# Kernel tuning notes

Hardware: AMD Instinct MI355X
Metric: run time of the kernel (lower is better)

Reference implementation:

```python
import jax, jax.numpy as jnp
import numpy as np

B, S, D, H, HD, L, W, MLP = 1, 4096, 1024, 16, 64, 3, 512, 4096
NB = S // W
EPS = 1e-5

def _layer_norm(x, g, b):
    m = jnp.mean(x, axis=-1, keepdims=True)
    v = jnp.mean(jnp.square(x - m), axis=-1, keepdims=True)
    return (x - m) * jax.lax.rsqrt(v + EPS) * g + b

def _rotate_half(x):
    x1, x2 = jnp.split(x, 2, axis=-1)
    return jnp.concatenate([-x2, x1], axis=-1)

def setup_inputs() -> dict:
    key = jax.random.key(0)
    ks = jax.random.split(key, 12)
    def nrm(k, shape):
        return jax.random.normal(k, shape, jnp.float32) * 0.02
    return {
        'hidden_states': jax.random.normal(ks[0], (B, S, D), jnp.float32),
        'position_ids': jnp.broadcast_to(jnp.arange(S, dtype=jnp.int32), (B, S)),
        'ln1_g': jnp.ones((L, D), jnp.float32), 'ln1_b': jnp.zeros((L, D), jnp.float32),
        'wq': nrm(ks[1], (L, D, D)), 'bq': jnp.zeros((L, D), jnp.float32),
        'wk': nrm(ks[2], (L, D, D)), 'bk': jnp.zeros((L, D), jnp.float32),
        'wv': nrm(ks[3], (L, D, D)), 'bv': jnp.zeros((L, D), jnp.float32),
        'wo': nrm(ks[4], (L, D, D)), 'bo': jnp.zeros((L, D), jnp.float32),
        'ln2_g': jnp.ones((L, D), jnp.float32), 'ln2_b': jnp.zeros((L, D), jnp.float32),
        'w1': nrm(ks[5], (L, D, MLP)), 'b1': jnp.zeros((L, MLP), jnp.float32),
        'w2': nrm(ks[6], (L, MLP, D)), 'b2': jnp.zeros((L, D), jnp.float32),
        'fln_g': jnp.ones((D,), jnp.float32), 'fln_b': jnp.zeros((D,), jnp.float32),
    }

def reference(hidden_states, position_ids, ln1_g, ln1_b, wq, bq, wk, bk, wv, bv,
              wo, bo, ln2_g, ln2_b, w1, b1, w2, b2, fln_g, fln_b):
    # RoPE tables (half-split / LLaMA convention)
    inv_freq = 1.0 / (10000.0 ** (jnp.arange(0, HD, 2, dtype=jnp.float32) / HD))
    ang = position_ids.astype(jnp.float32)[..., None] * inv_freq          # [B,S,HD/2]
    cos = jnp.concatenate([jnp.cos(ang)] * 2, axis=-1)[:, :, None, :]     # [B,S,1,HD]
    sin = jnp.concatenate([jnp.sin(ang)] * 2, axis=-1)[:, :, None, :]

    # causal sliding-window mask over (query-in-block, key-in-2-blocks)
    qi = jnp.arange(W)[:, None]
    kj = jnp.arange(2 * W)[None, :]
    rel = qi + W - kj                                                     # = i - j globally
    base = (rel >= 0) & (rel < W)                                         # [W,2W]
    valid = jnp.ones((NB, 2 * W), bool).at[0, :W].set(False)              # no keys before t=0
    mask = base[None, :, :] & valid[:, None, :]                           # [NB,W,2W]
    scale = HD ** -0.5

    x = hidden_states
    for l in range(L):
        h = _layer_norm(x, ln1_g[l], ln1_b[l])
        q = (h @ wq[l] + bq[l]).reshape(B, S, H, HD)
        k = (h @ wk[l] + bk[l]).reshape(B, S, H, HD)
        v = (h @ wv[l] + bv[l]).reshape(B, S, H, HD)
        q = q * cos + _rotate_half(q) * sin
        k = k * cos + _rotate_half(k) * sin
        qb = q.reshape(B, NB, W, H, HD)
        # keys/values for block b = [block b-1, block b] (pad one block in front)
        kp = jnp.pad(k, ((0, 0), (W, 0), (0, 0), (0, 0)))
        vp = jnp.pad(v, ((0, 0), (W, 0), (0, 0), (0, 0)))
        k2 = jnp.concatenate([kp[:, :-W].reshape(B, NB, W, H, HD),
                              kp[:, W:].reshape(B, NB, W, H, HD)], axis=2)  # [B,NB,2W,H,HD]
        v2 = jnp.concatenate([vp[:, :-W].reshape(B, NB, W, H, HD),
                              vp[:, W:].reshape(B, NB, W, H, HD)], axis=2)
        s = jnp.einsum('bnqhd,bnkhd->bnhqk', qb, k2) * scale              # [B,NB,H,W,2W]
        s = jnp.where(mask[None, :, None, :, :], s, -1e30)
        a = jax.nn.softmax(s, axis=-1)
        o = jnp.einsum('bnhqk,bnkhd->bnqhd', a, v2).reshape(B, S, D)
        x = x + (o @ wo[l] + bo[l])
        h = _layer_norm(x, ln2_g[l], ln2_b[l])
        m = jax.nn.gelu(h @ w1[l] + b1[l], approximate=False) @ w2[l] + b2[l]
        x = x + m
    return _layer_norm(x, fln_g, fln_b)
```

## Files before the change

### kernel.cpp

```cpp
#include <hip/hip_runtime.h>

typedef unsigned short u16;
typedef short s8v __attribute__((ext_vector_type(8)));
typedef float f4v __attribute__((ext_vector_type(4)));

__device__ __forceinline__ float bf2f(u16 u){ return __uint_as_float(((unsigned)u)<<16); }
__device__ __forceinline__ u16 f2bf(float f){
  unsigned u = __float_as_uint(f);
  unsigned r = u + 0x7fffu + ((u>>16)&1u);
  return (u16)(r>>16);
}
__device__ __forceinline__ void gload16(const void* g, void* l){
  __builtin_amdgcn_global_load_lds((const __attribute__((address_space(1))) void*)g,
                                   (__attribute__((address_space(3))) void*)l, 16, 0, 0);
}

struct TJobs {
  const float* src[18];
  u16* dst[18];
  int R[18];
  int C[18];
  int start[19];
};

__global__ __launch_bounds__(256) void transpose_pack(TJobs jb){
  __shared__ float tile[32][33];
  int bid = blockIdx.x;
  int j = 0;
  while (bid >= jb.start[j+1]) j++;
  int t = bid - jb.start[j];
  int C = jb.C[j], R = jb.R[j];
  int ctiles = C >> 5;
  int ty = t / ctiles, tx = t - ty*ctiles;
  const float* src = jb.src[j];
  u16* dst = jb.dst[j];
  int tid = threadIdx.x;
  #pragma unroll
  for (int i=0;i<4;i++){
    int e = tid*4 + i;
    int lr = e >> 5, lc = e & 31;
    tile[lr][lc] = src[(long)(ty*32+lr)*C + tx*32+lc];
  }
  __syncthreads();
  #pragma unroll
  for (int i=0;i<4;i++){
    int e = tid*4 + i;
    int lc = e >> 5, lr = e & 31;
    dst[(long)(tx*32+lc)*R + ty*32+lr] = f2bf(tile[lr][lc]);
  }
}

__global__ __launch_bounds__(256) void pack_bias(const float* __restrict__ bq, const float* __restrict__ bk,
                                                 const float* __restrict__ bv, float* __restrict__ outp){
  int t = blockIdx.x*256 + threadIdx.x;
  if (t >= 3*3072) return;
  int l = t / 3072, c = t - l*3072;
  float v = (c < 1024) ? bq[l*1024+c] : (c < 2048) ? bk[l*1024+c-1024] : bv[l*1024+c-2048];
  outp[t] = v;
}

__global__ __launch_bounds__(256) void rope_table(const int* __restrict__ pos, float* __restrict__ cosT,
                                                  float* __restrict__ sinT){
  int t = blockIdx.x*256 + threadIdx.x;
  int j = t & 31, s = t >> 5;
  float f = expf(-(float)j * 0.28782313662425572f);
  float ang = (float)pos[s] * f;
  cosT[t] = cosf(ang);
  sinT[t] = sinf(ang);
}

__global__ __launch_bounds__(256) void rope_apply(const u16* __restrict__ qkv, const float* __restrict__ cosT,
                                                  const float* __restrict__ sinT, u16* __restrict__ qr,
                                                  u16* __restrict__ kr, u16* __restrict__ vr){
  int t = blockIdx.x*256 + threadIdx.x;
  int j = t & 31, h = (t>>5) & 15, s = t >> 9;
  float c = cosT[(s<<5)+j], sn = sinT[(s<<5)+j];
  long base = (long)s*3072 + h*64 + j;
  long ob   = (long)s*1024 + h*64 + j;
  float q0 = bf2f(qkv[base]),      q1 = bf2f(qkv[base+32]);
  float k0 = bf2f(qkv[base+1024]), k1 = bf2f(qkv[base+1056]);
  qr[ob] = f2bf(q0*c - q1*sn);  qr[ob+32] = f2bf(q1*c + q0*sn);
  kr[ob] = f2bf(k0*c - k1*sn);  kr[ob+32] = f2bf(k1*c + k0*sn);
  vr[ob] = qkv[base+2048];      vr[ob+32] = qkv[base+2080];
}

__device__ __forceinline__ float block_sum(float v, float* red, int tid){
  #pragma unroll
  for (int m=1;m<64;m<<=1) v += __shfl_xor(v, m);
  int w = tid >> 6;
  if ((tid & 63) == 0) red[w] = v;
  __syncthreads();
  float r = red[0]+red[1]+red[2]+red[3];
  __syncthreads();
  return r;
}

template<int OUTF32>
__global__ __launch_bounds__(256) void ln_kernel(const float* __restrict__ x, const float* __restrict__ g,
                                                 const float* __restrict__ b, float* __restrict__ outF,
                                                 u16* __restrict__ outH){
  __shared__ float red[4];
  long row = blockIdx.x;
  int tid = threadIdx.x;
  const float4 xv = *reinterpret_cast<const float4*>(x + row*1024 + tid*4);
  float s = xv.x + xv.y + xv.z + xv.w;
  float mean = block_sum(s, red, tid) * (1.0f/1024.0f);
  float d0 = xv.x-mean, d1 = xv.y-mean, d2 = xv.z-mean, d3 = xv.w-mean;
  float ss = d0*d0 + d1*d1 + d2*d2 + d3*d3;
  float var = block_sum(ss, red, tid) * (1.0f/1024.0f);
  float rstd = rsqrtf(var + 1e-5f);
  int c = tid*4;
  const float4 gv = *reinterpret_cast<const float4*>(g + c);
  const float4 bv = *reinterpret_cast<const float4*>(b + c);
  float y0 = d0*rstd*gv.x + bv.x, y1 = d1*rstd*gv.y + bv.y;
  float y2 = d2*rstd*gv.z + bv.z, y3 = d3*rstd*gv.w + bv.w;
  if (OUTF32){
    float4 o; o.x=y0; o.y=y1; o.z=y2; o.w=y3;
    *reinterpret_cast<float4*>(outF + row*1024 + c) = o;
  } else {
    outH[row*1024 + c+0] = f2bf(y0);
    outH[row*1024 + c+1] = f2bf(y1);
    outH[row*1024 + c+2] = f2bf(y2);
    outH[row*1024 + c+3] = f2bf(y3);
  }
}

template<int EPI>
__global__ __launch_bounds__(512, 2) void gemm256(const u16* __restrict__ A, const u16* __restrict__ BT,
                                                  const float* __restrict__ bias,
                                                  u16* __restrict__ outH, int N, int K){
  __shared__ u16 LA[2][16384];
  __shared__ u16 LB[2][16384];
  const int tid = threadIdx.x;
  const int gx = N >> 8;
  const int cpx = gridDim.x >> 3;
  const int sbid = (blockIdx.x & 7) * cpx + (blockIdx.x >> 3);
  const int bn = sbid % gx, bm = sbid / gx;
  const int w = tid >> 6, lane = tid & 63;
  const int wr = w >> 2, wc = w & 3;
  const int l15 = lane & 15, lg = lane >> 4;

  const int srow = tid >> 3;
  const int c16s = (tid & 7) ^ (srow & 7);
  const u16* gA0 = A  + (long)(bm*256 + srow)*K + c16s*8;
  const u16* gB0 = BT + (long)(bn*256 + srow)*K + c16s*8;
  const long j64K = (long)64*K;
  const int ldst = tid*8;

  f4v acc[8][4];
  #pragma unroll
  for (int i=0;i<8;i++)
    #pragma unroll
    for (int j=0;j<4;j++)
      acc[i][j] = (f4v){0.f,0.f,0.f,0.f};

  const int swz = (l15 & 7);
  const int cA0 = ((0*4 + lg) ^ swz) * 8;
  const int cA1 = ((1*4 + lg) ^ swz) * 8;

  #define STAGE(buf, k0) do { \
    _Pragma("unroll") \
    for (int j=0;j<4;j++) gload16(gA0 + (long)j*j64K + (k0), &LA[buf][j*4096 + ldst]); \
    _Pragma("unroll") \
    for (int j=0;j<4;j++) gload16(gB0 + (long)j*j64K + (k0), &LB[buf][j*4096 + ldst]); \
  } while(0)

  const int nt = K >> 6;
  STAGE(0, 0);
  STAGE(1, 64);
  asm volatile("s_waitcnt vmcnt(8)" ::: "memory");
  __builtin_amdgcn_s_barrier();
  __builtin_amdgcn_sched_barrier(0);

  for (int t = 0; t < nt; ++t){
    const int buf = t & 1;
    s8v bfr[4][2];
    #pragma unroll
    for (int nf=0;nf<4;nf++){
      const int rb = (wc*64 + nf*16 + l15)*64;
      bfr[nf][0] = *(const s8v*)&LB[buf][rb + cA0];
      bfr[nf][1] = *(const s8v*)&LB[buf][rb + cA1];
    }
    #pragma unroll
    for (int half=0; half<2; ++half){
      s8v af[4][2];
      #pragma unroll
      for (int mi=0;mi<4;mi++){
        const int ra = (wr*128 + half*64 + mi*16 + l15)*64;
        af[mi][0] = *(const s8v*)&LA[buf][ra + cA0];
        af[mi][1] = *(const s8v*)&LA[buf][ra + cA1];
      }
      __builtin_amdgcn_s_setprio(1);
      #pragma unroll
      for (int mi=0;mi<4;mi++)
        #pragma unroll
        for (int nf=0;nf<4;nf++){
          acc[half*4+mi][nf] = __builtin_amdgcn_mfma_f32_16x16x32_bf16(af[mi][0], bfr[nf][0], acc[half*4+mi][nf], 0,0,0);
          acc[half*4+mi][nf] = __builtin_amdgcn_mfma_f32_16x16x32_bf16(af[mi][1], bfr[nf][1], acc[half*4+mi][nf], 0,0,0);
        }
      __builtin_amdgcn_s_setprio(0);
    }
    __builtin_amdgcn_sched_barrier(0);
    __builtin_amdgcn_s_barrier();
    __builtin_amdgcn_sched_barrier(0);
    if (t + 2 < nt){
      STAGE(buf, (t+2) << 6);
      asm volatile("s_waitcnt vmcnt(8)" ::: "memory");
    } else {
      asm volatile("s_waitcnt vmcnt(0)" ::: "memory");
    }
    __builtin_amdgcn_s_barrier();
    __builtin_amdgcn_sched_barrier(0);
  }
  #undef STAGE

  #pragma unroll
  for (int mi=0;mi<8;mi++){
    int row = bm*256 + wr*128 + mi*16 + lg*4;
    #pragma unroll
    for (int nf=0;nf<4;nf++){
      int col = bn*256 + wc*64 + nf*16 + l15;
      float bcol = bias[col];
      #pragma unroll
      for (int r=0;r<4;r++){
        float v = acc[mi][nf][r] + bcol;
        long idx = (long)(row + r)*N + col;
        if (EPI == 0){
          outH[idx] = f2bf(v);
        } else {
          float gl = 0.5f*v*(1.0f + erff(v*0.70710678118654752f));
          outH[idx] = f2bf(gl);
        }
      }
    }
  }
}

template<int EPI>
__global__ __launch_bounds__(256) void gemm_bt(const u16* __restrict__ A, const u16* __restrict__ BT,
                                               const float* __restrict__ bias, const float* __restrict__ resid,
                                               float* __restrict__ outF, u16* __restrict__ outH,
                                               int M, int N, int K){
  __shared__ u16 As[2][4096];
  __shared__ u16 Bs[2][4096];
  const int tid = threadIdx.x;
  const int gx = N >> 7;
  const int nwg = gridDim.x;
  const int cpx = nwg >> 3;
  const int sbid = (blockIdx.x & 7) * cpx + (blockIdx.x >> 3);
  const int bn = sbid % gx, bm = sbid / gx;

  const int w = tid >> 6, lane = tid & 63;
  const int wr = w >> 1, wc = w & 1;
  const int l15 = lane & 15, k8 = (lane >> 4) * 8;

  f4v acc[4][4];
  #pragma unroll
  for (int i=0;i<4;i++)
    #pragma unroll
    for (int j=0;j<4;j++)
      acc[i][j] = (f4v){0.f,0.f,0.f,0.f};

  const int fe = tid * 8;
  const int r0 = fe >> 5, c0 = fe & 31;
  const u16* ga0 = A  + ((long)(bm*128 + r0))*K + c0;
  const u16* gb0 = BT + ((long)(bn*128 + r0))*K + c0;
  const u16* ga1 = ga0 + (long)64*K;
  const u16* gb1 = gb0 + (long)64*K;

  const int nt = K >> 5;
  gload16(ga0, &As[0][fe]);
  gload16(ga1, &As[0][fe + 2048]);
  gload16(gb0, &Bs[0][fe]);
  gload16(gb1, &Bs[0][fe + 2048]);
  __syncthreads();

  int cur = 0;
  for (int t = 0; t < nt; ++t){
    if (t + 1 < nt){
      const int kn = (t + 1) << 5;
      gload16(ga0 + kn, &As[cur^1][fe]);
      gload16(ga1 + kn, &As[cur^1][fe + 2048]);
      gload16(gb0 + kn, &Bs[cur^1][fe]);
      gload16(gb1 + kn, &Bs[cur^1][fe + 2048]);
    }
    s8v af[4], bfr[4];
    #pragma unroll
    for (int i=0;i<4;i++){
      af[i]  = *(const s8v*)&As[cur][(wr*64 + i*16 + l15)*32 + k8];
      bfr[i] = *(const s8v*)&Bs[cur][(wc*64 + i*16 + l15)*32 + k8];
    }
    #pragma unroll
    for (int mi=0;mi<4;mi++)
      #pragma unroll
      for (int nf=0;nf<4;nf++)
        acc[mi][nf] = __builtin_amdgcn_mfma_f32_16x16x32_bf16(af[mi], bfr[nf], acc[mi][nf], 0, 0, 0);
    __syncthreads();
    cur ^= 1;
  }

  const int r4 = (lane >> 4) * 4;
  #pragma unroll
  for (int mi=0;mi<4;mi++){
    int row = bm*128 + wr*64 + mi*16 + r4;
    #pragma unroll
    for (int nf=0;nf<4;nf++){
      int col = bn*128 + wc*64 + nf*16 + l15;
      float bcol = bias[col];
      #pragma unroll
      for (int r=0;r<4;r++){
        float v = acc[mi][nf][r] + bcol;
        long idx = (long)(row + r)*N + col;
        if (EPI == 0){
          outH[idx] = f2bf(v);
        } else if (EPI == 1){
          outF[idx] = resid[idx] + v;
        } else {
          float gl = 0.5f*v*(1.0f + erff(v*0.70710678118654752f));
          outH[idx] = f2bf(gl);
        }
      }
    }
  }
}

__global__ __launch_bounds__(256) void attn_kernel(const u16* __restrict__ qr, const u16* __restrict__ kr,
                                                   const u16* __restrict__ vr, u16* __restrict__ ao){
  __shared__ u16 Pl[4][1280];
  __shared__ u16 Vl[4][2304];
  const int tid = threadIdx.x, w = tid >> 6, lane = tid & 63;
  const int task = blockIdx.x*4 + w;
  const int head = task >> 7;
  const int q0 = (task & 127) * 32;
  const int l15 = lane & 15, lg = lane >> 4, k8 = lg * 8;

  s8v aq[2][2];
  #pragma unroll
  for (int mi=0;mi<2;mi++)
    #pragma unroll
    for (int kf=0;kf<2;kf++)
      aq[mi][kf] = *(const s8v*)&qr[(long)(q0 + mi*16 + l15)*1024 + head*64 + kf*32 + k8];

  f4v o[2][4];
  #pragma unroll
  for (int i=0;i<2;i++)
    #pragma unroll
    for (int j=0;j<4;j++)
      o[i][j] = (f4v){0.f,0.f,0.f,0.f};
  float mrun[2][4], lrun[2][4];
  #pragma unroll
  for (int i=0;i<2;i++)
    #pragma unroll
    for (int r=0;r<4;r++){ mrun[i][r] = -1e30f; lrun[i][r] = 0.f; }

  const int ktlo = (q0 >= 512) ? ((q0 - 511) >> 5) : 0;
  const int kthi = (q0 + 31) >> 5;

  for (int kt = ktlo; kt <= kthi; ++kt){
    const int k0 = kt * 32;
    #pragma unroll
    for (int t=0;t<4;t++){
      int e = t*64 + lane;
      int r = e >> 3, c8 = (e & 7) * 8;
      *(s8v*)&Vl[w][r*72 + c8] = *(const s8v*)&vr[(long)(k0 + r)*1024 + head*64 + c8];
    }
    s8v bk[2][2];
    #pragma unroll
    for (int nf=0;nf<2;nf++)
      #pragma unroll
      for (int kf=0;kf<2;kf++)
        bk[nf][kf] = *(const s8v*)&kr[(long)(k0 + nf*16 + l15)*1024 + head*64 + kf*32 + k8];
    f4v s[2][2];
    #pragma unroll
    for (int mi=0;mi<2;mi++)
      #pragma unroll
      for (int nf=0;nf<2;nf++){
        f4v z = (f4v){0.f,0.f,0.f,0.f};
        z = __builtin_amdgcn_mfma_f32_16x16x32_bf16(aq[mi][0], bk[nf][0], z, 0,0,0);
        z = __builtin_amdgcn_mfma_f32_16x16x32_bf16(aq[mi][1], bk[nf][1], z, 0,0,0);
        s[mi][nf] = z;
      }
    float alpha[2][4];
    #pragma unroll
    for (int mi=0;mi<2;mi++){
      #pragma unroll
      for (int r=0;r<4;r++){
        int q = q0 + mi*16 + lg*4 + r;
        int kk0 = k0 + l15, kk1 = k0 + 16 + l15;
        bool ok0 = (kk0 <= q) && (q - kk0 < 512);
        bool ok1 = (kk1 <= q) && (q - kk1 < 512);
        float sv0 = ok0 ? s[mi][0][r]*0.125f : -1e30f;
        float sv1 = ok1 ? s[mi][1][r]*0.125f : -1e30f;
        float tm = fmaxf(sv0, sv1);
        tm = fmaxf(tm, __shfl_xor(tm, 1));
        tm = fmaxf(tm, __shfl_xor(tm, 2));
        tm = fmaxf(tm, __shfl_xor(tm, 4));
        tm = fmaxf(tm, __shfl_xor(tm, 8));
        float mnew = fmaxf(mrun[mi][r], tm);
        float al = __expf(mrun[mi][r] - mnew);
        float p0 = ok0 ? __expf(sv0 - mnew) : 0.f;
        float p1 = ok1 ? __expf(sv1 - mnew) : 0.f;
        float rs = p0 + p1;
        rs += __shfl_xor(rs, 1);
        rs += __shfl_xor(rs, 2);
        rs += __shfl_xor(rs, 4);
        rs += __shfl_xor(rs, 8);
        mrun[mi][r] = mnew;
        lrun[mi][r] = lrun[mi][r]*al + rs;
        alpha[mi][r] = al;
        s[mi][0][r] = p0;
        s[mi][1][r] = p1;
      }
      #pragma unroll
      for (int df=0;df<4;df++)
        #pragma unroll
        for (int r=0;r<4;r++)
          o[mi][df][r] *= alpha[mi][r];
    }
    #pragma unroll
    for (int mi=0;mi<2;mi++)
      #pragma unroll
      for (int nf=0;nf<2;nf++)
        #pragma unroll
        for (int r=0;r<4;r++)
          Pl[w][(mi*16 + lg*4 + r)*40 + nf*16 + l15] = f2bf(s[mi][nf][r]);
    s8v ap[2];
    #pragma unroll
    for (int mi=0;mi<2;mi++)
      ap[mi] = *(const s8v*)&Pl[w][(mi*16 + l15)*40 + k8];
    s8v bv[4];
    #pragma unroll
    for (int df=0;df<4;df++){
      #pragma unroll
      for (int i=0;i<8;i++)
        bv[df][i] = (short)Vl[w][(k8 + i)*72 + df*16 + l15];
    }
    #pragma unroll
    for (int mi=0;mi<2;mi++)
      #pragma unroll
      for (int df=0;df<4;df++)
        o[mi][df] = __builtin_amdgcn_mfma_f32_16x16x32_bf16(ap[mi], bv[df], o[mi][df], 0,0,0);
  }
  #pragma unroll
  for (int mi=0;mi<2;mi++)
    #pragma unroll
    for (int df=0;df<4;df++)
      #pragma unroll
      for (int r=0;r<4;r++){
        long row = q0 + mi*16 + lg*4 + r;
        int col = head*64 + df*16 + l15;
        ao[row*1024 + col] = f2bf(o[mi][df][r] / lrun[mi][r]);
      }
}

extern "C" void kernel_launch(void* const* d_in, const int* in_sizes, int n_in,
                              void* d_out, int out_size, void* d_ws, size_t ws_size,
                              hipStream_t stream){
  const float* hidden = (const float*)d_in[0];
  const int*   pos    = (const int*)d_in[1];
  const float* ln1_g  = (const float*)d_in[2];
  const float* ln1_b  = (const float*)d_in[3];
  const float* wq     = (const float*)d_in[4];
  const float* bq     = (const float*)d_in[5];
  const float* wk     = (const float*)d_in[6];
  const float* bk     = (const float*)d_in[7];
  const float* wv     = (const float*)d_in[8];
  const float* bv     = (const float*)d_in[9];
  const float* wo     = (const float*)d_in[10];
  const float* bo     = (const float*)d_in[11];
  const float* ln2_g  = (const float*)d_in[12];
  const float* ln2_b  = (const float*)d_in[13];
  const float* w1     = (const float*)d_in[14];
  const float* b1     = (const float*)d_in[15];
  const float* w2     = (const float*)d_in[16];
  const float* b2     = (const float*)d_in[17];
  const float* fg     = (const float*)d_in[18];
  const float* fb     = (const float*)d_in[19];
  float* out = (float*)d_out;

  char* ws = (char*)d_ws;
  size_t off = 0;
  auto alloc = [&](size_t bytes)->char*{
    char* p = ws + off;
    off = (off + bytes + 255) & ~(size_t)255;
    return p;
  };
  u16*   WQKVT = (u16*)  alloc(3ull*3072*1024*2);
  u16*   WOT   = (u16*)  alloc(3ull*1024*1024*2);
  u16*   W1T   = (u16*)  alloc(3ull*4096*1024*2);
  u16*   W2T   = (u16*)  alloc(3ull*1024*4096*2);
  float* BQKV  = (float*)alloc(3ull*3072*4);
  float* COS   = (float*)alloc(4096ull*32*4);
  float* SIN   = (float*)alloc(4096ull*32*4);
  float* X     = (float*)alloc(4096ull*1024*4);
  u16*   HB    = (u16*)  alloc(4096ull*1024*2);
  u16*   QKV   = (u16*)  alloc(4096ull*3072*2);
  u16*   QR    = (u16*)  alloc(4096ull*1024*2);
  u16*   KR    = (u16*)  alloc(4096ull*1024*2);
  u16*   VR    = (u16*)  alloc(4096ull*1024*2);
  u16*   AO    = (u16*)  alloc(4096ull*1024*2);
  u16*   MB    = (u16*)  alloc(4096ull*4096*2);

  TJobs jb;
  int total = 0, ji = 0;
  for (int l=0;l<3;l++){
    const float* srcs[6] = { wq + (size_t)l*1024*1024, wk + (size_t)l*1024*1024, wv + (size_t)l*1024*1024,
                             wo + (size_t)l*1024*1024, w1 + (size_t)l*1024*4096, w2 + (size_t)l*4096*1024 };
    u16* dsts[6] = { WQKVT + (size_t)l*3072*1024, WQKVT + (size_t)l*3072*1024 + 1024*1024,
                     WQKVT + (size_t)l*3072*1024 + 2048*1024, WOT + (size_t)l*1024*1024,
                     W1T + (size_t)l*4096*1024, W2T + (size_t)l*1024*4096 };
    int Rs[6] = {1024,1024,1024,1024,1024,4096};
    int Cs[6] = {1024,1024,1024,1024,4096,1024};
    for (int k=0;k<6;k++){
      jb.src[ji] = srcs[k]; jb.dst[ji] = dsts[k]; jb.R[ji] = Rs[k]; jb.C[ji] = Cs[k];
      jb.start[ji] = total;
      total += (Rs[k]/32)*(Cs[k]/32);
      ji++;
    }
  }
  jb.start[18] = total;

  transpose_pack<<<total, 256, 0, stream>>>(jb);
  pack_bias<<<36, 256, 0, stream>>>(bq, bk, bv, BQKV);
  rope_table<<<512, 256, 0, stream>>>(pos, COS, SIN);

  for (int l=0;l<3;l++){
    const float* xin = (l == 0) ? hidden : X;
    ln_kernel<0><<<4096, 256, 0, stream>>>(xin, ln1_g + l*1024, ln1_b + l*1024, nullptr, HB);
    gemm256<0><<<12*16, 512, 0, stream>>>(HB, WQKVT + (size_t)l*3072*1024, BQKV + l*3072,
                                          QKV, 3072, 1024);
    rope_apply<<<8192, 256, 0, stream>>>(QKV, COS, SIN, QR, KR, VR);
    attn_kernel<<<512, 256, 0, stream>>>(QR, KR, VR, AO);
    gemm_bt<1><<<8*32, 256, 0, stream>>>(AO, WOT + (size_t)l*1024*1024, bo + l*1024,
                                         xin, X, nullptr, 4096, 1024, 1024);
    ln_kernel<0><<<4096, 256, 0, stream>>>(X, ln2_g + l*1024, ln2_b + l*1024, nullptr, HB);
    gemm256<2><<<16*16, 512, 0, stream>>>(HB, W1T + (size_t)l*4096*1024, b1 + l*4096,
                                          MB, 4096, 1024);
    gemm_bt<1><<<8*32, 256, 0, stream>>>(MB, W2T + (size_t)l*1024*4096, b2 + l*1024,
                                         X, X, nullptr, 4096, 1024, 4096);
  }
  ln_kernel<1><<<4096, 256, 0, stream>>>(X, fg, fb, out, nullptr);
}
```

Before: 1.023 ms.

## Interleave next-tile global-to-LDS loads with quadrant MFMA phases in gemm256

The K loop of the 256x256 GEMM is restructured into four MFMA phases, one per quadrant of each wave's 128x64 output tile. The global-to-LDS loads for the next B tile and the tile-after-next A tile are issued in pieces between these phases, each separated by barriers. The old scheme did all compute, then a barrier, then a full stage load and wait. The goal is to overlap memory traffic with matrix-core work and shorten the per-iteration stall. In exchange it adds more barriers per iteration, and the final iterations issue redundant clamped loads that leave loads outstanding at kernel end.

```diff
diff --git a/kernel.cpp b/kernel.cpp
--- a/kernel.cpp
+++ b/kernel.cpp
@@ -142,10 +142,18 @@
 
   const int srow = tid >> 3;
   const int c16s = (tid & 7) ^ (srow & 7);
-  const u16* gA0 = A  + (long)(bm*256 + srow)*K + c16s*8;
-  const u16* gB0 = BT + (long)(bn*256 + srow)*K + c16s*8;
-  const long j64K = (long)64*K;
+  const u16* gAb = A  + (long)(bm*256)*K + c16s*8;
+  const u16* gBb = BT + (long)(bn*256)*K + c16s*8;
   const int ldst = tid*8;
+
+  #define STGA(bf, rb, k0) do{ \
+    gload16(gAb + (long)((rb) + srow)*K + (k0),      &LA[bf][(rb)*64 + ldst]); \
+    gload16(gAb + (long)((rb) + 64 + srow)*K + (k0), &LA[bf][(rb)*64 + 4096 + ldst]); \
+  }while(0)
+  #define STGB(bf, rb, k0) do{ \
+    gload16(gBb + (long)((rb) + srow)*K + (k0),      &LB[bf][(rb)*64 + ldst]); \
+    gload16(gBb + (long)((rb) + 64 + srow)*K + (k0), &LB[bf][(rb)*64 + 4096 + ldst]); \
+  }while(0)
 
   f4v acc[8][4];
   #pragma unroll
@@ -154,65 +162,104 @@
     for (int j=0;j<4;j++)
       acc[i][j] = (f4v){0.f,0.f,0.f,0.f};
 
-  const int swz = (l15 & 7);
-  const int cA0 = ((0*4 + lg) ^ swz) * 8;
-  const int cA1 = ((1*4 + lg) ^ swz) * 8;
-
-  #define STAGE(buf, k0) do { \
-    _Pragma("unroll") \
-    for (int j=0;j<4;j++) gload16(gA0 + (long)j*j64K + (k0), &LA[buf][j*4096 + ldst]); \
-    _Pragma("unroll") \
-    for (int j=0;j<4;j++) gload16(gB0 + (long)j*j64K + (k0), &LB[buf][j*4096 + ldst]); \
-  } while(0)
+  const int swz = l15 & 7;
+  const int cs0 = ((0 + lg) ^ swz) * 8;
+  const int cs1 = ((4 + lg) ^ swz) * 8;
 
   const int nt = K >> 6;
-  STAGE(0, 0);
-  STAGE(1, 64);
-  asm volatile("s_waitcnt vmcnt(8)" ::: "memory");
+  STGA(0, 0,   0);  STGA(0, 128, 0);
+  STGB(0, 0,   0);  STGB(0, 128, 0);
+  STGA(1, 0,   64); STGA(1, 128, 64);
+  asm volatile("s_waitcnt vmcnt(4)" ::: "memory");
   __builtin_amdgcn_s_barrier();
-  __builtin_amdgcn_sched_barrier(0);
 
   for (int t = 0; t < nt; ++t){
     const int buf = t & 1;
-    s8v bfr[4][2];
-    #pragma unroll
-    for (int nf=0;nf<4;nf++){
+    const int n1 = (t+1 < nt) ? t+1 : nt-1;
+    const int n2 = (t+2 < nt) ? t+2 : nt-1;
+    const int b1 = n1 & 1, b2 = n2 & 1;
+    const int k1 = n1 << 6, k2 = n2 << 6;
+
+    s8v a0[4][2], a1[4][2], bfr[4][2];
+    #pragma unroll
+    for (int mi=0;mi<4;mi++){
+      const int ra = (wr*128 + mi*16 + l15)*64;
+      a0[mi][0] = *(const s8v*)&LA[buf][ra + cs0];
+      a0[mi][1] = *(const s8v*)&LA[buf][ra + cs1];
+    }
+    #pragma unroll
+    for (int nf=0;nf<2;nf++){
       const int rb = (wc*64 + nf*16 + l15)*64;
-      bfr[nf][0] = *(const s8v*)&LB[buf][rb + cA0];
-      bfr[nf][1] = *(const s8v*)&LB[buf][rb + cA1];
-    }
-    #pragma unroll
-    for (int half=0; half<2; ++half){
-      s8v af[4][2];
-      #pragma unroll
-      for (int mi=0;mi<4;mi++){
-        const int ra = (wr*128 + half*64 + mi*16 + l15)*64;
-        af[mi][0] = *(const s8v*)&LA[buf][ra + cA0];
-        af[mi][1] = *(const s8v*)&LA[buf][ra + cA1];
-      }
-      __builtin_amdgcn_s_setprio(1);
-      #pragma unroll
-      for (int mi=0;mi<4;mi++)
-        #pragma unroll
-        for (int nf=0;nf<4;nf++){
-          acc[half*4+mi][nf] = __builtin_amdgcn_mfma_f32_16x16x32_bf16(af[mi][0], bfr[nf][0], acc[half*4+mi][nf], 0,0,0);
-          acc[half*4+mi][nf] = __builtin_amdgcn_mfma_f32_16x16x32_bf16(af[mi][1], bfr[nf][1], acc[half*4+mi][nf], 0,0,0);
-        }
-      __builtin_amdgcn_s_setprio(0);
-    }
-    __builtin_amdgcn_sched_barrier(0);
-    __builtin_amdgcn_s_barrier();
-    __builtin_amdgcn_sched_barrier(0);
-    if (t + 2 < nt){
-      STAGE(buf, (t+2) << 6);
-      asm volatile("s_waitcnt vmcnt(8)" ::: "memory");
-    } else {
-      asm volatile("s_waitcnt vmcnt(0)" ::: "memory");
-    }
-    __builtin_amdgcn_s_barrier();
-    __builtin_amdgcn_sched_barrier(0);
-  }
-  #undef STAGE
+      bfr[nf][0] = *(const s8v*)&LB[buf][rb + cs0];
+      bfr[nf][1] = *(const s8v*)&LB[buf][rb + cs1];
+    }
+    STGB(b1, 0, k1);
+    __builtin_amdgcn_s_barrier();
+    __builtin_amdgcn_s_setprio(1);
+    #pragma unroll
+    for (int mi=0;mi<4;mi++)
+      #pragma unroll
+      for (int nf=0;nf<2;nf++){
+        acc[mi][nf] = __builtin_amdgcn_mfma_f32_16x16x32_bf16(a0[mi][0], bfr[nf][0], acc[mi][nf], 0,0,0);
+        acc[mi][nf] = __builtin_amdgcn_mfma_f32_16x16x32_bf16(a0[mi][1], bfr[nf][1], acc[mi][nf], 0,0,0);
+      }
+    __builtin_amdgcn_s_setprio(0);
+    __builtin_amdgcn_s_barrier();
+
+    #pragma unroll
+    for (int nf=2;nf<4;nf++){
+      const int rb = (wc*64 + nf*16 + l15)*64;
+      bfr[nf][0] = *(const s8v*)&LB[buf][rb + cs0];
+      bfr[nf][1] = *(const s8v*)&LB[buf][rb + cs1];
+    }
+    #pragma unroll
+    for (int mi=0;mi<4;mi++){
+      const int ra = (wr*128 + 64 + mi*16 + l15)*64;
+      a1[mi][0] = *(const s8v*)&LA[buf][ra + cs0];
+      a1[mi][1] = *(const s8v*)&LA[buf][ra + cs1];
+    }
+    STGB(b1, 128, k1);
+    __builtin_amdgcn_s_barrier();
+    __builtin_amdgcn_s_setprio(1);
+    #pragma unroll
+    for (int mi=0;mi<4;mi++)
+      #pragma unroll
+      for (int nf=2;nf<4;nf++){
+        acc[mi][nf] = __builtin_amdgcn_mfma_f32_16x16x32_bf16(a0[mi][0], bfr[nf][0], acc[mi][nf], 0,0,0);
+        acc[mi][nf] = __builtin_amdgcn_mfma_f32_16x16x32_bf16(a0[mi][1], bfr[nf][1], acc[mi][nf], 0,0,0);
+      }
+    __builtin_amdgcn_s_setprio(0);
+    __builtin_amdgcn_s_barrier();
+
+    STGA(b2, 0, k2);
+    __builtin_amdgcn_s_barrier();
+    __builtin_amdgcn_s_setprio(1);
+    #pragma unroll
+    for (int mi=0;mi<4;mi++)
+      #pragma unroll
+      for (int nf=0;nf<2;nf++){
+        acc[4+mi][nf] = __builtin_amdgcn_mfma_f32_16x16x32_bf16(a1[mi][0], bfr[nf][0], acc[4+mi][nf], 0,0,0);
+        acc[4+mi][nf] = __builtin_amdgcn_mfma_f32_16x16x32_bf16(a1[mi][1], bfr[nf][1], acc[4+mi][nf], 0,0,0);
+      }
+    __builtin_amdgcn_s_setprio(0);
+    __builtin_amdgcn_s_barrier();
+
+    STGA(b2, 128, k2);
+    asm volatile("s_waitcnt vmcnt(4)" ::: "memory");
+    __builtin_amdgcn_s_barrier();
+    __builtin_amdgcn_s_setprio(1);
+    #pragma unroll
+    for (int mi=0;mi<4;mi++)
+      #pragma unroll
+      for (int nf=2;nf<4;nf++){
+        acc[4+mi][nf] = __builtin_amdgcn_mfma_f32_16x16x32_bf16(a1[mi][0], bfr[nf][0], acc[4+mi][nf], 0,0,0);
+        acc[4+mi][nf] = __builtin_amdgcn_mfma_f32_16x16x32_bf16(a1[mi][1], bfr[nf][1], acc[4+mi][nf], 0,0,0);
+      }
+    __builtin_amdgcn_s_setprio(0);
+    __builtin_amdgcn_s_barrier();
+  }
+  #undef STGA
+  #undef STGB
 
   #pragma unroll
   for (int mi=0;mi<8;mi++){
```

Measured after the change: 1.084 ms. 1.06x slower.
